# Kernel optimization log

Hardware: AMD Instinct MI355X
Metric: run time of the kernel (lower is better)

The kernel has to match this reference:

```python
import jax, jax.numpy as jnp
import numpy as np

DIM = 192
HEADS = 4
EPS = 1e-12  # F.normalize default eps


def setup_inputs() -> dict:
    key = jax.random.key(0)
    ks = jax.random.split(key, 5)
    b, c, h, w = 8, DIM, 128, 128
    x = jax.random.normal(ks[0], (b, c, h, w), dtype=jnp.float32)
    w_qkv = jax.random.normal(ks[1], (3 * DIM, DIM, 1, 1), dtype=jnp.float32) * (1.0 / np.sqrt(DIM))
    w_dw = jax.random.normal(ks[2], (3 * DIM, 1, 3, 3), dtype=jnp.float32) * (1.0 / 3.0)
    w_proj = jax.random.normal(ks[3], (DIM, DIM, 1, 1), dtype=jnp.float32) * (1.0 / np.sqrt(DIM))
    temperature = jnp.ones((HEADS, 1, 1), dtype=jnp.float32)
    return {"x": x, "w_qkv": w_qkv, "w_dw": w_dw, "w_proj": w_proj, "temperature": temperature}


def _conv1x1(x, w):
    # x: [b,c,h,w], w: [o,c,1,1] -> [b,o,h,w]
    return jnp.einsum('bchw,oc->bohw', x, w[:, :, 0, 0])


def _dwconv3x3(x, w):
    # depthwise 3x3, padding=1; x: [b,C,h,w], w: [C,1,3,3]
    C = x.shape[1]
    return jax.lax.conv_general_dilated(
        x, w, window_strides=(1, 1), padding=((1, 1), (1, 1)),
        dimension_numbers=('NCHW', 'OIHW', 'NCHW'), feature_group_count=C)


def _l2norm(x):
    n = jnp.linalg.norm(x, axis=-1, keepdims=True)
    return x / jnp.maximum(n, EPS)


def reference(x, w_qkv, w_dw, w_proj, temperature):
    b, c, h, w = x.shape
    head = HEADS
    ch = c // head  # channels per head
    qkv = _dwconv3x3(_conv1x1(x, w_qkv), w_dw)  # [b, 3c, h, w]
    q, k, v = jnp.split(qkv, 3, axis=1)  # each [b, c, h, w]

    def to_heads(t):
        # b (head ch) h w -> b head h (ch w)
        t = t.reshape(b, head, ch, h, w)
        return t.transpose(0, 1, 3, 2, 4).reshape(b, head, h, ch * w)

    q1 = _l2norm(to_heads(q))
    k1 = _l2norm(to_heads(k))
    v1 = to_heads(v)
    # attn over height dim: [b, head, h, h]
    attn = jax.nn.softmax(jnp.einsum('bhif,bhjf->bhij', q1, k1) * temperature[None], axis=-1)
    out = jnp.einsum('bhij,bhjf->bhif', attn, v1)  # [b, head, h, ch*w]
    # b head h (ch w) -> b (head ch) h w
    out = out.reshape(b, head, h, ch, w).transpose(0, 1, 3, 2, 4).reshape(b, c, h, w)
    return _conv1x1(out, w_proj)
```

## Files before the change

kernel.cpp:

```cpp
#include <hip/hip_runtime.h>
#include <hip/hip_bf16.h>

#define BB 8
#define CC 192
#define C3 576
#define NH 4
#define CH 48
#define HH 128
#define WW 128
#define HW 16384
#define FF 6144

typedef short s16x8 __attribute__((ext_vector_type(8)));
typedef float f32x4 __attribute__((ext_vector_type(4)));

constexpr size_t SPM = 32ull * 128 * 128;

constexpr size_t OFF_XT  = 0;
constexpr size_t SZ_XT   = (size_t)BB * HW * CC * 2;
constexpr size_t OFF_WQ  = OFF_XT + SZ_XT;
constexpr size_t SZ_WQ   = (size_t)C3 * CC * 2;
constexpr size_t OFF_WP  = OFF_WQ + SZ_WQ;
constexpr size_t SZ_WP   = (size_t)CC * CC * 2;
constexpr size_t OFF_RAW = OFF_WP + SZ_WP;
constexpr size_t SZ_RAW  = (size_t)BB * C3 * HW * 2;
constexpr size_t OFF_DW  = OFF_RAW + SZ_RAW;
constexpr size_t OFF_SP  = OFF_DW + SZ_RAW;
constexpr size_t OFF_ATB = OFF_SP + 8 * SPM * 4;
constexpr size_t OFF_RQ  = OFF_ATB + 32ull * 128 * 128 * 2;
constexpr size_t OFF_RK  = OFF_RQ + 32 * 128 * 4;
constexpr size_t OFF_PS  = OFF_SP;

__device__ __forceinline__ short bf16bits(float v) {
  __hip_bfloat16 t = __float2bfloat16(v);
  return *reinterpret_cast<short*>(&t);
}
__device__ __forceinline__ float b2f(short u) {
  union { unsigned int i; float f; } x;
  x.i = ((unsigned int)(unsigned short)u) << 16;
  return x.f;
}

__device__ __forceinline__ void gload16(const void* g, void* l) {
  __builtin_amdgcn_global_load_lds((const __attribute__((address_space(1))) unsigned int*)g,
                                   (__attribute__((address_space(3))) unsigned int*)l, 16, 0, 0);
}

#define VMWAIT(N) asm volatile("s_waitcnt vmcnt(" #N ")" ::: "memory")
__device__ __forceinline__ void vmdrain() { asm volatile("s_waitcnt vmcnt(0)" ::: "memory"); }
__device__ __forceinline__ void ldsbar() {
  asm volatile("s_waitcnt lgkmcnt(0)" ::: "memory");
  __builtin_amdgcn_s_barrier();
}

__global__ __launch_bounds__(256) void k_cvt_t(const float* __restrict__ in,
                                               __hip_bfloat16* __restrict__ outT) {
  const int p0 = blockIdx.x * 64;
  const int c0 = blockIdx.y * 32;
  const int b = blockIdx.z;
  __shared__ float t[32][65];
  const float* ib = in + (size_t)b * CC * HW;
  const int tid = threadIdx.x;
  {
    const int c = tid >> 3, pl = (tid & 7) * 8;
    const float* s = ib + (size_t)(c0 + c) * HW + p0 + pl;
#pragma unroll
    for (int j = 0; j < 8; ++j) t[c][pl + j] = s[j];
  }
  __syncthreads();
  {
    const int pl = tid >> 2, cl = (tid & 3) * 8;
    __hip_bfloat16* d = outT + (size_t)b * HW * CC + (size_t)(p0 + pl) * CC + c0 + cl;
#pragma unroll
    for (int j = 0; j < 8; ++j) d[j] = __float2bfloat16(t[cl + j][pl]);
  }
}

__global__ __launch_bounds__(256) void k_cvt_w2(const float* __restrict__ in1, int n1,
                                                const float* __restrict__ in2, int n2,
                                                __hip_bfloat16* __restrict__ out) {
  const int i = blockIdx.x * 256 + threadIdx.x;
  if (i < n1) out[i] = __float2bfloat16(in1[i]);
  else if (i < n1 + n2) out[i] = __float2bfloat16(in2[i - n1]);
}

__global__ __launch_bounds__(256) void k_gemm(const __hip_bfloat16* __restrict__ xT,
                                              const __hip_bfloat16* __restrict__ Wb,
                                              __hip_bfloat16* __restrict__ out) {
  const int pG = blockIdx.x * 4;
  const int mBase = blockIdx.y * 96;
  const int b = blockIdx.z;
  __shared__ char smem[62976];
  const int tid = threadIdx.x, wave = tid >> 6, lane = tid & 63;
  const int wm = wave >> 1, wn = wave & 1;
  const __hip_bfloat16* xb = xT + (size_t)b * HW * CC;
  char* Bbase = smem + 36864;

#pragma unroll
  for (int it = 0; it < 9; ++it) {
    const int s = it * 256 + tid;
    const int kc = s / 384, ci = s % 384;
    const int row = ci & 15, kg = (ci >> 4) & 3, mf = ci >> 6;
    gload16(Wb + (size_t)(mBase + mf * 16 + row) * CC + kc * 32 + kg * 8,
            smem + it * 4096 + wave * 1024);
  }

  auto stageB = [&](int pt, int kc, int buf) {
    char* Blc = Bbase + buf * 8192;
    const int pBase = (pG + pt) * 128;
#pragma unroll
    for (int is = 0; is < 2; ++is) {
      const int ci = is * 256 + tid;
      const int col = ci & 15, kg = (ci >> 4) & 3, nf = ci >> 6;
      gload16(xb + (size_t)(pBase + nf * 16 + col) * CC + kc * 32 + kg * 8,
              Blc + is * 4096 + wave * 1024);
    }
  };

  short* E = (short*)Bbase;
  const int r0 = (lane >> 4) * 4, cl = lane & 15;

  for (int pt = 0; pt < 4; ++pt) {
    stageB(pt, 0, 0);
    stageB(pt, 1, 1);
    f32x4 acc[3][4] = {};
#pragma unroll
    for (int kc = 0; kc < 6; ++kc) {
      if (kc < 4) stageB(pt, kc + 2, (kc + 2) % 3);
      if (kc < 4) VMWAIT(4);
      else if (kc == 4) VMWAIT(2);
      else VMWAIT(0);
      __builtin_amdgcn_s_barrier();
      char* Alc = smem + kc * 6144;
      char* Blc = Bbase + (kc % 3) * 8192;
      s16x8 a[3], bf[4];
#pragma unroll
      for (int i = 0; i < 3; ++i) a[i] = *(const s16x8*)(Alc + ((wm * 3 + i) << 10) + (lane << 4));
#pragma unroll
      for (int j = 0; j < 4; ++j) bf[j] = *(const s16x8*)(Blc + ((wn * 4 + j) << 10) + (lane << 4));
#pragma unroll
      for (int i = 0; i < 3; ++i)
#pragma unroll
        for (int j = 0; j < 4; ++j)
          acc[i][j] = __builtin_amdgcn_mfma_f32_16x16x32_bf16(a[i], bf[j], acc[i][j], 0, 0, 0);
      __builtin_amdgcn_s_barrier();
    }
#pragma unroll
    for (int i = 0; i < 3; ++i) {
      const int lr = wm * 48 + i * 16 + r0;
#pragma unroll
      for (int j = 0; j < 4; ++j) {
        const int col = (wn * 4 + j) * 16 + cl;
#pragma unroll
        for (int r = 0; r < 4; ++r) E[(lr + r) * 136 + col] = bf16bits(acc[i][j][r]);
      }
    }
    ldsbar();
    __hip_bfloat16* ob = out + (size_t)b * C3 * HW + (pG + pt) * 128;
#pragma unroll
    for (int it = 0; it < 6; ++it) {
      const int vi = it * 256 + tid;
      const int row = vi >> 4, c8 = (vi & 15) * 8;
      const s16x8 v = *(const s16x8*)(E + row * 136 + c8);
      *(s16x8*)(ob + (size_t)(mBase + row) * HW + c8) = v;
    }
    ldsbar();
  }
}

__global__ __launch_bounds__(256) void k_dwconv(const __hip_bfloat16* __restrict__ in,
                                                const float* __restrict__ wdw,
                                                __hip_bfloat16* __restrict__ out,
                                                __hip_bfloat16* __restrict__ vt,
                                                float* __restrict__ psum) {
  const int c = blockIdx.x;
  const int b = blockIdx.z;
  __shared__ __hip_bfloat16 IN[2][34][152];
  __shared__ char TR[8192];
  const int tid = threadIdx.x;
  const __hip_bfloat16* src = in + ((size_t)b * C3 + c) * HW;
  const bool isV = (c >= 2 * CC);
  if (tid < 136) {
    const int bz = tid >= 68, t2 = tid - bz * 68;
    const int r = t2 >> 1, col = (t2 & 1) ? 136 : 0;
    *(s16x8*)(&IN[bz][r][col]) = (s16x8){};
  }
  const float* wp = wdw + c * 9;
  float wgt[9];
#pragma unroll
  for (int q = 0; q < 9; ++q) wgt[q] = wp[q];

  s16x8 ld[3];
  auto loadTile = [&](int h0) {
#pragma unroll
    for (int it = 0; it < 3; ++it) {
      const int vi = it * 256 + tid;
      if (vi < 544) {
        const int r = vi >> 4, w8 = vi & 15;
        const int hg = h0 - 1 + r;
        s16x8 v = {};
        if (hg >= 0 && hg < HH) v = *(const s16x8*)(src + (size_t)hg * WW + w8 * 8);
        ld[it] = v;
      }
    }
  };
  auto writeTile = [&](int buf) {
#pragma unroll
    for (int it = 0; it < 3; ++it) {
      const int vi = it * 256 + tid;
      if (vi < 544) {
        const int r = vi >> 4, w8 = vi & 15;
        *(s16x8*)(&IN[buf][r][8 + w8 * 8]) = ld[it];
      }
    }
  };

  loadTile(0);
  writeTile(0);
  __syncthreads();

  const int hl = tid >> 3, w0 = (tid & 7) * 16;
  for (int t = 0; t < 4; ++t) {
    const int h0 = t * 32;
    const int cur = t & 1;
    if (t < 3) loadTile(h0 + 32);
    float res[16] = {};
#pragma unroll
    for (int dh = 0; dh < 3; ++dh) {
      const __hip_bfloat16* rp = &IN[cur][hl + dh][0];
      const s16x8 v0 = *(const s16x8*)(rp + w0);
      const s16x8 v1 = *(const s16x8*)(rp + w0 + 8);
      const s16x8 v2 = *(const s16x8*)(rp + w0 + 16);
      const s16x8 v3 = *(const s16x8*)(rp + w0 + 24);
      float rv[18];
      rv[0] = b2f(v0[7]);
#pragma unroll
      for (int e = 0; e < 8; ++e) rv[1 + e] = b2f(v1[e]);
#pragma unroll
      for (int e = 0; e < 8; ++e) rv[9 + e] = b2f(v2[e]);
      rv[17] = b2f(v3[0]);
      const float wa = wgt[dh * 3], wb = wgt[dh * 3 + 1], wc = wgt[dh * 3 + 2];
#pragma unroll
      for (int ww = 0; ww < 16; ++ww)
        res[ww] += rv[ww] * wa + rv[ww + 1] * wb + rv[ww + 2] * wc;
    }
    if (!isV) {
      short pk[16];
#pragma unroll
      for (int ww = 0; ww < 16; ++ww) pk[ww] = bf16bits(res[ww]);
      __hip_bfloat16* dst = out + ((size_t)b * C3 + c) * HW + (size_t)(h0 + hl) * WW + w0;
      *(s16x8*)dst = *(const s16x8*)pk;
      *(s16x8*)(dst + 8) = *(const s16x8*)(pk + 8);
      float ss = 0.f;
#pragma unroll
      for (int ww = 0; ww < 16; ++ww) ss += res[ww] * res[ww];
#pragma unroll
      for (int off = 4; off > 0; off >>= 1) ss += __shfl_down(ss, off);
      if ((tid & 7) == 0) psum[((size_t)b * HH + h0 + hl) * 384 + c] = ss;
      if (t < 3) writeTile(cur ^ 1);
      __syncthreads();
    } else {
      const int rel = c - 2 * CC;
      const int hd = rel / CH, ch = rel - hd * CH;
#pragma unroll
      for (int ww = 0; ww < 16; ++ww) {
        const int w = w0 + ww;
        const int blk = ((w << 2) + (hl >> 3)) ^ ((w >> 3) & 3);
        *(short*)(TR + (blk << 4) + ((hl & 7) << 1)) = bf16bits(res[ww]);
      }
      __syncthreads();
      const int w = tid >> 1, hf = tid & 1;
      short ot[16];
#pragma unroll
      for (int j = 0; j < 2; ++j) {
        const int hh = hf * 16 + j * 8;
        const int blk = ((w << 2) + (hh >> 3)) ^ ((w >> 3) & 3);
        *(s16x8*)(ot + j * 8) = *(const s16x8*)(TR + (blk << 4));
      }
      __hip_bfloat16* vd = vt + ((size_t)(b * NH + hd) * FF + (size_t)ch * WW + w) * HH + h0 + hf * 16;
      *(s16x8*)vd = *(const s16x8*)ot;
      *(s16x8*)(vd + 8) = *(const s16x8*)(ot + 8);
      if (t < 3) writeTile(cur ^ 1);
      __syncthreads();
    }
  }
}

__global__ __launch_bounds__(64) void k_norms2(const float* __restrict__ psum,
                                               float* __restrict__ rq, float* __restrict__ rk) {
  const int i = blockIdx.x;
  const int hd = blockIdx.y;
  const int b = blockIdx.z & 7;
  const int which = blockIdx.z >> 3;
  const int lane = threadIdx.x;
  float s = 0.f;
  if (lane < 48) s = psum[((size_t)b * HH + i) * 384 + which * CC + hd * CH + lane];
#pragma unroll
  for (int off = 32; off > 0; off >>= 1) s += __shfl_down(s, off);
  if (lane == 0) {
    const float n = sqrtf(s);
    float* dst = which ? rk : rq;
    dst[(b * NH + hd) * HH + i] = 1.f / fmaxf(n, 1e-12f);
  }
}

__global__ __launch_bounds__(256) void k_qkm(const __hip_bfloat16* __restrict__ dw,
                                             float* __restrict__ sp) {
  const int ks = blockIdx.x;
  const int bh = blockIdx.y;
  const int i0 = blockIdx.z * 64;
  const int b = bh >> 2, hd = bh & 3;
  const __hip_bfloat16* qb = dw + ((size_t)b * C3 + hd * CH) * HW;
  const __hip_bfloat16* kb = dw + ((size_t)b * C3 + CC + hd * CH) * HW;
  __shared__ char smem[36864];
  const int tid = threadIdx.x, wave = tid >> 6, lane = tid & 63;
  const int wm = wave >> 1, wn = wave & 1;
  f32x4 acc[2][4] = {};

  auto stage = [&](int chunk, int buf) {
    const int ch = ks * 6 + (chunk >> 2);
    const int w0 = (chunk & 3) * 32;
    char* Alc = smem + buf * 12288;
    char* Blc = Alc + 4096;
    {
      const int row = tid & 15, kg = (tid >> 4) & 3;
      gload16(qb + (size_t)ch * HW + (i0 + (tid >> 6) * 16 + row) * WW + w0 + kg * 8,
              Alc + wave * 1024);
    }
#pragma unroll
    for (int is = 0; is < 2; ++is) {
      const int ci = is * 256 + tid;
      const int col = ci & 15, kg = (ci >> 4) & 3, nf = ci >> 6;
      gload16(kb + (size_t)ch * HW + (nf * 16 + col) * WW + w0 + kg * 8,
              Blc + is * 4096 + wave * 1024);
    }
  };

  stage(0, 0);
  stage(1, 1);
  for (int chunk = 0; chunk < 24; ++chunk) {
    if (chunk < 22) stage(chunk + 2, (chunk + 2) % 3);
    if (chunk < 22) VMWAIT(6);
    else if (chunk == 22) VMWAIT(3);
    else VMWAIT(0);
    __builtin_amdgcn_s_barrier();
    char* Alc = smem + (chunk % 3) * 12288;
    char* Blc = Alc + 4096;
    s16x8 a[2], bf[4];
#pragma unroll
    for (int i = 0; i < 2; ++i) a[i] = *(const s16x8*)(Alc + ((wm * 2 + i) << 10) + (lane << 4));
#pragma unroll
    for (int j = 0; j < 4; ++j) bf[j] = *(const s16x8*)(Blc + ((wn * 4 + j) << 10) + (lane << 4));
#pragma unroll
    for (int i = 0; i < 2; ++i)
#pragma unroll
      for (int j = 0; j < 4; ++j)
        acc[i][j] = __builtin_amdgcn_mfma_f32_16x16x32_bf16(a[i], bf[j], acc[i][j], 0, 0, 0);
    __builtin_amdgcn_s_barrier();
  }
  float* o = sp + (size_t)ks * SPM + (size_t)bh * HH * HH;
  const int r0 = (lane >> 4) * 4, cl = lane & 15;
#pragma unroll
  for (int i = 0; i < 2; ++i)
#pragma unroll
    for (int j = 0; j < 4; ++j) {
      const int ii = i0 + wm * 32 + i * 16 + r0;
      const int jj = wn * 64 + j * 16 + cl;
#pragma unroll
      for (int r = 0; r < 4; ++r) o[(ii + r) * HH + jj] = acc[i][j][r];
    }
}

__global__ __launch_bounds__(256) void k_softmax(const float* __restrict__ sp,
                                                 const float* __restrict__ rq,
                                                 const float* __restrict__ rk,
                                                 const float* __restrict__ temp,
                                                 __hip_bfloat16* __restrict__ atb) {
  const int wave = threadIdx.x >> 6, lane = threadIdx.x & 63;
  const int i = blockIdx.x * 4 + wave;
  const int bh = blockIdx.y;
  const int hd = bh & 3;
  const size_t rowoff = ((size_t)bh * HH + i) * HH;
  float s0 = 0.f, s1 = 0.f;
#pragma unroll
  for (int ks = 0; ks < 8; ++ks) {
    s0 += sp[ks * SPM + rowoff + lane];
    s1 += sp[ks * SPM + rowoff + lane + 64];
  }
  const float scale = rq[bh * HH + i] * temp[hd];
  s0 *= scale * rk[bh * HH + lane];
  s1 *= scale * rk[bh * HH + lane + 64];
  float m = fmaxf(s0, s1);
#pragma unroll
  for (int off = 32; off > 0; off >>= 1) m = fmaxf(m, __shfl_xor(m, off));
  const float e0 = expf(s0 - m), e1 = expf(s1 - m);
  float ssum = e0 + e1;
#pragma unroll
  for (int off = 32; off > 0; off >>= 1) ssum += __shfl_xor(ssum, off);
  const float inv = 1.f / ssum;
  atb[rowoff + lane] = __float2bfloat16(e0 * inv);
  atb[rowoff + lane + 64] = __float2bfloat16(e1 * inv);
}

__global__ __launch_bounds__(256) void k_pvm(const __hip_bfloat16* __restrict__ atb,
                                             const __hip_bfloat16* __restrict__ vt,
                                             __hip_bfloat16* __restrict__ pvout) {
  const int fs0 = blockIdx.x * 2;
  const int bh = blockIdx.y;
  const __hip_bfloat16* ab = atb + (size_t)bh * HH * HH;
  __shared__ char smem[57344];
  const int tid = threadIdx.x, wave = tid >> 6, lane = tid & 63;
  const int wm = wave >> 1, wn = wave & 1;

#pragma unroll
  for (int it = 0; it < 8; ++it) {
    const int s = it * 256 + tid;
    const int kc = s >> 9, ci = s & 511;
    const int row = ci & 15, kg = (ci >> 4) & 3, mf = ci >> 6;
    gload16(ab + (size_t)(mf * 16 + row) * HH + kc * 32 + kg * 8,
            smem + it * 4096 + wave * 1024);
  }
  char* Bbase = smem + 32768;

  auto stageB = [&](int st, int buf) {
    const int fs = fs0 + (st >> 2);
    const int kj0 = (st & 3) * 32;
    const __hip_bfloat16* vb = vt + ((size_t)bh * FF + fs * 128) * HH;
    char* Blc = Bbase + buf * 8192;
#pragma unroll
    for (int is = 0; is < 2; ++is) {
      const int ci = is * 256 + tid;
      const int col = ci & 15, kg = (ci >> 4) & 3, nf = ci >> 6;
      gload16(vb + (size_t)(nf * 16 + col) * HH + kj0 + kg * 8,
              Blc + is * 4096 + wave * 1024);
    }
  };

  stageB(0, 0);
  stageB(1, 1);
  const int r0 = (lane >> 4) * 4, cl = lane & 15;
  for (int fr = 0; fr < 2; ++fr) {
    f32x4 acc[4][4] = {};
#pragma unroll
    for (int kc = 0; kc < 4; ++kc) {
      const int st = fr * 4 + kc;
      if (st < 6) stageB(st + 2, (st + 2) % 3);
      if (st < 6) VMWAIT(4);
      else if (st == 6) VMWAIT(2);
      else VMWAIT(0);
      __builtin_amdgcn_s_barrier();
      char* Alc = smem + kc * 8192;
      char* Blc = Bbase + (st % 3) * 8192;
      s16x8 a[4], bf[4];
#pragma unroll
      for (int i = 0; i < 4; ++i) a[i] = *(const s16x8*)(Alc + ((wm * 4 + i) << 10) + (lane << 4));
#pragma unroll
      for (int j = 0; j < 4; ++j) bf[j] = *(const s16x8*)(Blc + ((wn * 4 + j) << 10) + (lane << 4));
#pragma unroll
      for (int i = 0; i < 4; ++i)
#pragma unroll
        for (int j = 0; j < 4; ++j)
          acc[i][j] = __builtin_amdgcn_mfma_f32_16x16x32_bf16(a[i], bf[j], acc[i][j], 0, 0, 0);
      __builtin_amdgcn_s_barrier();
    }
    __hip_bfloat16* ob = pvout + (size_t)bh * HH * FF;
    const int fs = fs0 + fr;
#pragma unroll
    for (int i = 0; i < 4; ++i)
#pragma unroll
      for (int j = 0; j < 4; ++j) {
        const int ii = wm * 64 + i * 16 + r0;
        const int f = fs * 128 + (wn * 4 + j) * 16 + cl;
#pragma unroll
        for (int r = 0; r < 4; ++r) ob[(size_t)(ii + r) * FF + f] = __float2bfloat16(acc[i][j][r]);
      }
  }
}

__global__ __launch_bounds__(256) void k_proj(const __hip_bfloat16* __restrict__ pv,
                                              const __hip_bfloat16* __restrict__ Wp,
                                              float* __restrict__ out) {
  const int i = blockIdx.x;
  const int b = blockIdx.y;
  __shared__ __hip_bfloat16 Al[6144];
  __shared__ __hip_bfloat16 Braw[12288];
  __shared__ __hip_bfloat16 Bfrag[4096];
  char* Alc = (char*)Al;
  char* Brc = (char*)Braw;
  char* Bfc = (char*)Bfrag;
  const int tid = threadIdx.x, wave = tid >> 6, lane = tid & 63;
  const int wm = wave >> 1, wn = wave & 1;
  f32x4 acc[6][4] = {};
  for (int hf = 0; hf < 2; ++hf) {
    if (hf) __syncthreads();
#pragma unroll
    for (int it = 0; it < 6; ++it) {
      const int vi = it * 256 + tid;
      const int r = vi >> 4, w8 = vi & 15;
      const int hi = (r >= 48) ? 1 : 0;
      const int hd = hf * 2 + hi, ch = r - hi * 48;
      const s16x8 v = *(const s16x8*)(pv + ((size_t)(b * NH + hd) * HH + i) * FF + ch * 128 + w8 * 8);
      *(s16x8*)(Brc + r * 256 + ((w8 ^ (r & 15)) << 4)) = v;
    }
    __syncthreads();
    for (int kc = 0; kc < 3; ++kc) {
      const int c0 = hf * 96 + kc * 32;
#pragma unroll
      for (int is = 0; is < 3; ++is) {
        const int ci = is * 256 + tid;
        const int row = ci & 15, kg = (ci >> 4) & 3, mf = ci >> 6;
        gload16(Wp + (size_t)(mf * 16 + row) * CC + c0 + kg * 8,
                Alc + is * 4096 + wave * 1024);
      }
#pragma unroll
      for (int it = 0; it < 2; ++it) {
        const int vi = it * 256 + tid;
        const int col = vi & 15, kg = (vi >> 4) & 3, nf = vi >> 6;
        const int w = nf * 16 + col;
        short tmp[8];
#pragma unroll
        for (int e = 0; e < 8; ++e) {
          const int r = (kc * 4 + kg) * 8 + e;
          tmp[e] = *(const short*)(Brc + r * 256 + (((w >> 3) ^ (r & 15)) << 4) + (w & 7) * 2);
        }
        *(s16x8*)(Bfc + ((nf * 64 + kg * 16 + col) << 4)) = *(const s16x8*)tmp;
      }
      vmdrain();
      __syncthreads();
      s16x8 a[6], bf[4];
#pragma unroll
      for (int mi = 0; mi < 6; ++mi)
        a[mi] = *(const s16x8*)(Alc + ((wm * 6 + mi) << 10) + (lane << 4));
#pragma unroll
      for (int j = 0; j < 4; ++j)
        bf[j] = *(const s16x8*)(Bfc + (((wn * 4 + j) * 64 + lane) << 4));
#pragma unroll
      for (int mi = 0; mi < 6; ++mi)
#pragma unroll
        for (int j = 0; j < 4; ++j)
          acc[mi][j] = __builtin_amdgcn_mfma_f32_16x16x32_bf16(a[mi], bf[j], acc[mi][j], 0, 0, 0);
      __syncthreads();
    }
  }
  const int r0 = (lane >> 4) * 4, cl = lane & 15;
#pragma unroll
  for (int mi = 0; mi < 6; ++mi) {
    const int o = (wm * 6 + mi) * 16 + r0;
#pragma unroll
    for (int j = 0; j < 4; ++j) {
      const int w = (wn * 4 + j) * 16 + cl;
      float* dst = out + ((size_t)b * CC + o) * HW + i * 128 + w;
#pragma unroll
      for (int r = 0; r < 4; ++r) dst[(size_t)r * HW] = acc[mi][j][r];
    }
  }
}

extern "C" void kernel_launch(void* const* d_in, const int* in_sizes, int n_in,
                              void* d_out, int out_size, void* d_ws, size_t ws_size,
                              hipStream_t stream) {
  const float* x     = (const float*)d_in[0];
  const float* wqkv  = (const float*)d_in[1];
  const float* wdw   = (const float*)d_in[2];
  const float* wproj = (const float*)d_in[3];
  const float* temp  = (const float*)d_in[4];

  char* ws = (char*)d_ws;
  __hip_bfloat16* xTb    = (__hip_bfloat16*)(ws + OFF_XT);
  __hip_bfloat16* vt     = (__hip_bfloat16*)(ws + OFF_XT);
  __hip_bfloat16* Wq     = (__hip_bfloat16*)(ws + OFF_WQ);
  __hip_bfloat16* Wp     = (__hip_bfloat16*)(ws + OFF_WP);
  __hip_bfloat16* qkvraw = (__hip_bfloat16*)(ws + OFF_RAW);
  __hip_bfloat16* pvout  = (__hip_bfloat16*)(ws + OFF_RAW);
  __hip_bfloat16* qkvdw  = (__hip_bfloat16*)(ws + OFF_DW);
  float* sp    = (float*)(ws + OFF_SP);
  float* psum  = (float*)(ws + OFF_PS);
  __hip_bfloat16* atb = (__hip_bfloat16*)(ws + OFF_ATB);
  float* rq    = (float*)(ws + OFF_RQ);
  float* rk    = (float*)(ws + OFF_RK);

  k_cvt_w2<<<dim3((C3 * CC + CC * CC + 255) / 256), 256, 0, stream>>>(wqkv, C3 * CC, wproj, CC * CC, Wq);
  k_cvt_t<<<dim3(HW / 64, CC / 32, BB), 256, 0, stream>>>(x, xTb);
  k_gemm<<<dim3(HW / 512, C3 / 96, BB), 256, 0, stream>>>(xTb, Wq, qkvraw);
  k_dwconv<<<dim3(C3, 1, BB), 256, 0, stream>>>(qkvraw, wdw, qkvdw, vt, psum);
  k_norms2<<<dim3(HH, NH, 2 * BB), 64, 0, stream>>>(psum, rq, rk);
  k_qkm<<<dim3(8, 32, 2), 256, 0, stream>>>(qkvdw, sp);
  k_softmax<<<dim3(HH / 4, 32), 256, 0, stream>>>(sp, rq, rk, temp, atb);
  k_pvm<<<dim3(24, 32), 256, 0, stream>>>(atb, vt, pvout);
  k_proj<<<dim3(HH, BB), 256, 0, stream>>>(pvout, Wp, (float*)d_out);
}
```

Measured before the change: 259.2 us.

## Shrink GEMM LDS footprint and split dwconv over row tiles per block

The GEMM moves from triple to double buffering of B tiles and writes its epilogue in two halves, reducing shared memory from about 62KB to 52KB so more blocks can fit per CU. The depthwise conv kernel now launches one block per 32-row tile instead of looping over four tiles with software prefetch. This gives four times more blocks and a smaller LDS footprint. In exchange, the GEMM loses a stage of prefetch depth and the conv loses its load/compute overlap inside each block, and halo rows are reloaded from global memory.

```diff
diff --git a/kernel.cpp b/kernel.cpp
--- a/kernel.cpp
+++ b/kernel.cpp
@@ -90,7 +90,7 @@
   const int pG = blockIdx.x * 4;
   const int mBase = blockIdx.y * 96;
   const int b = blockIdx.z;
-  __shared__ char smem[62976];
+  __shared__ char smem[53248];
   const int tid = threadIdx.x, wave = tid >> 6, lane = tid & 63;
   const int wm = wave >> 1, wn = wave & 1;
   const __hip_bfloat16* xb = xT + (size_t)b * HW * CC;
@@ -122,17 +122,15 @@
 
   for (int pt = 0; pt < 4; ++pt) {
     stageB(pt, 0, 0);
-    stageB(pt, 1, 1);
     f32x4 acc[3][4] = {};
 #pragma unroll
     for (int kc = 0; kc < 6; ++kc) {
-      if (kc < 4) stageB(pt, kc + 2, (kc + 2) % 3);
-      if (kc < 4) VMWAIT(4);
-      else if (kc == 4) VMWAIT(2);
+      if (kc < 5) stageB(pt, kc + 1, (kc + 1) & 1);
+      if (kc < 5) VMWAIT(2);
       else VMWAIT(0);
       __builtin_amdgcn_s_barrier();
       char* Alc = smem + kc * 6144;
-      char* Blc = Bbase + (kc % 3) * 8192;
+      char* Blc = Bbase + (kc & 1) * 8192;
       s16x8 a[3], bf[4];
 #pragma unroll
       for (int i = 0; i < 3; ++i) a[i] = *(const s16x8*)(Alc + ((wm * 3 + i) << 10) + (lane << 4));
@@ -145,26 +143,31 @@
           acc[i][j] = __builtin_amdgcn_mfma_f32_16x16x32_bf16(a[i], bf[j], acc[i][j], 0, 0, 0);
       __builtin_amdgcn_s_barrier();
     }
-#pragma unroll
-    for (int i = 0; i < 3; ++i) {
-      const int lr = wm * 48 + i * 16 + r0;
-#pragma unroll
-      for (int j = 0; j < 4; ++j) {
-        const int col = (wn * 4 + j) * 16 + cl;
-#pragma unroll
-        for (int r = 0; r < 4; ++r) E[(lr + r) * 136 + col] = bf16bits(acc[i][j][r]);
+    __hip_bfloat16* ob = out + (size_t)b * C3 * HW + (pG + pt) * 128;
+#pragma unroll
+    for (int half = 0; half < 2; ++half) {
+      if (wm == half) {
+#pragma unroll
+        for (int i = 0; i < 3; ++i) {
+          const int lr = i * 16 + r0;
+#pragma unroll
+          for (int j = 0; j < 4; ++j) {
+            const int col = (wn * 4 + j) * 16 + cl;
+#pragma unroll
+            for (int r = 0; r < 4; ++r) E[(lr + r) * 136 + col] = bf16bits(acc[i][j][r]);
+          }
+        }
       }
-    }
-    ldsbar();
-    __hip_bfloat16* ob = out + (size_t)b * C3 * HW + (pG + pt) * 128;
-#pragma unroll
-    for (int it = 0; it < 6; ++it) {
-      const int vi = it * 256 + tid;
-      const int row = vi >> 4, c8 = (vi & 15) * 8;
-      const s16x8 v = *(const s16x8*)(E + row * 136 + c8);
-      *(s16x8*)(ob + (size_t)(mBase + row) * HW + c8) = v;
-    }
-    ldsbar();
+      ldsbar();
+#pragma unroll
+      for (int it = 0; it < 3; ++it) {
+        const int vi = it * 256 + tid;
+        const int row = vi >> 4, c8 = (vi & 15) * 8;
+        const s16x8 v = *(const s16x8*)(E + row * 136 + c8);
+        *(s16x8*)(ob + (size_t)(mBase + half * 48 + row) * HW + c8) = v;
+      }
+      ldsbar();
+    }
   }
 }
 
@@ -173,116 +176,89 @@
                                                 __hip_bfloat16* __restrict__ out,
                                                 __hip_bfloat16* __restrict__ vt,
                                                 float* __restrict__ psum) {
-  const int c = blockIdx.x;
+  const int h0 = blockIdx.x * 32;
+  const int c = blockIdx.y;
   const int b = blockIdx.z;
-  __shared__ __hip_bfloat16 IN[2][34][152];
+  __shared__ __hip_bfloat16 IN[34][152];
   __shared__ char TR[8192];
   const int tid = threadIdx.x;
   const __hip_bfloat16* src = in + ((size_t)b * C3 + c) * HW;
-  const bool isV = (c >= 2 * CC);
-  if (tid < 136) {
-    const int bz = tid >= 68, t2 = tid - bz * 68;
-    const int r = t2 >> 1, col = (t2 & 1) ? 136 : 0;
-    *(s16x8*)(&IN[bz][r][col]) = (s16x8){};
+  if (tid < 68) {
+    const int r = tid >> 1, col = (tid & 1) ? 136 : 0;
+    *(s16x8*)(&IN[r][col]) = (s16x8){};
+  }
+#pragma unroll
+  for (int it = 0; it < 3; ++it) {
+    const int vi = it * 256 + tid;
+    if (vi < 544) {
+      const int r = vi >> 4, w8 = vi & 15;
+      const int hg = h0 - 1 + r;
+      s16x8 v = {};
+      if (hg >= 0 && hg < HH) v = *(const s16x8*)(src + (size_t)hg * WW + w8 * 8);
+      *(s16x8*)(&IN[r][8 + w8 * 8]) = v;
+    }
   }
   const float* wp = wdw + c * 9;
   float wgt[9];
 #pragma unroll
   for (int q = 0; q < 9; ++q) wgt[q] = wp[q];
-
-  s16x8 ld[3];
-  auto loadTile = [&](int h0) {
-#pragma unroll
-    for (int it = 0; it < 3; ++it) {
-      const int vi = it * 256 + tid;
-      if (vi < 544) {
-        const int r = vi >> 4, w8 = vi & 15;
-        const int hg = h0 - 1 + r;
-        s16x8 v = {};
-        if (hg >= 0 && hg < HH) v = *(const s16x8*)(src + (size_t)hg * WW + w8 * 8);
-        ld[it] = v;
-      }
-    }
-  };
-  auto writeTile = [&](int buf) {
-#pragma unroll
-    for (int it = 0; it < 3; ++it) {
-      const int vi = it * 256 + tid;
-      if (vi < 544) {
-        const int r = vi >> 4, w8 = vi & 15;
-        *(s16x8*)(&IN[buf][r][8 + w8 * 8]) = ld[it];
-      }
-    }
-  };
-
-  loadTile(0);
-  writeTile(0);
   __syncthreads();
 
   const int hl = tid >> 3, w0 = (tid & 7) * 16;
-  for (int t = 0; t < 4; ++t) {
-    const int h0 = t * 32;
-    const int cur = t & 1;
-    if (t < 3) loadTile(h0 + 32);
-    float res[16] = {};
-#pragma unroll
-    for (int dh = 0; dh < 3; ++dh) {
-      const __hip_bfloat16* rp = &IN[cur][hl + dh][0];
-      const s16x8 v0 = *(const s16x8*)(rp + w0);
-      const s16x8 v1 = *(const s16x8*)(rp + w0 + 8);
-      const s16x8 v2 = *(const s16x8*)(rp + w0 + 16);
-      const s16x8 v3 = *(const s16x8*)(rp + w0 + 24);
-      float rv[18];
-      rv[0] = b2f(v0[7]);
-#pragma unroll
-      for (int e = 0; e < 8; ++e) rv[1 + e] = b2f(v1[e]);
-#pragma unroll
-      for (int e = 0; e < 8; ++e) rv[9 + e] = b2f(v2[e]);
-      rv[17] = b2f(v3[0]);
-      const float wa = wgt[dh * 3], wb = wgt[dh * 3 + 1], wc = wgt[dh * 3 + 2];
-#pragma unroll
-      for (int ww = 0; ww < 16; ++ww)
-        res[ww] += rv[ww] * wa + rv[ww + 1] * wb + rv[ww + 2] * wc;
-    }
-    if (!isV) {
-      short pk[16];
-#pragma unroll
-      for (int ww = 0; ww < 16; ++ww) pk[ww] = bf16bits(res[ww]);
-      __hip_bfloat16* dst = out + ((size_t)b * C3 + c) * HW + (size_t)(h0 + hl) * WW + w0;
-      *(s16x8*)dst = *(const s16x8*)pk;
-      *(s16x8*)(dst + 8) = *(const s16x8*)(pk + 8);
-      float ss = 0.f;
-#pragma unroll
-      for (int ww = 0; ww < 16; ++ww) ss += res[ww] * res[ww];
-#pragma unroll
-      for (int off = 4; off > 0; off >>= 1) ss += __shfl_down(ss, off);
-      if ((tid & 7) == 0) psum[((size_t)b * HH + h0 + hl) * 384 + c] = ss;
-      if (t < 3) writeTile(cur ^ 1);
-      __syncthreads();
-    } else {
-      const int rel = c - 2 * CC;
-      const int hd = rel / CH, ch = rel - hd * CH;
-#pragma unroll
-      for (int ww = 0; ww < 16; ++ww) {
-        const int w = w0 + ww;
-        const int blk = ((w << 2) + (hl >> 3)) ^ ((w >> 3) & 3);
-        *(short*)(TR + (blk << 4) + ((hl & 7) << 1)) = bf16bits(res[ww]);
-      }
-      __syncthreads();
-      const int w = tid >> 1, hf = tid & 1;
-      short ot[16];
-#pragma unroll
-      for (int j = 0; j < 2; ++j) {
-        const int hh = hf * 16 + j * 8;
-        const int blk = ((w << 2) + (hh >> 3)) ^ ((w >> 3) & 3);
-        *(s16x8*)(ot + j * 8) = *(const s16x8*)(TR + (blk << 4));
-      }
-      __hip_bfloat16* vd = vt + ((size_t)(b * NH + hd) * FF + (size_t)ch * WW + w) * HH + h0 + hf * 16;
-      *(s16x8*)vd = *(const s16x8*)ot;
-      *(s16x8*)(vd + 8) = *(const s16x8*)(ot + 8);
-      if (t < 3) writeTile(cur ^ 1);
-      __syncthreads();
-    }
+  float res[16] = {};
+#pragma unroll
+  for (int dh = 0; dh < 3; ++dh) {
+    const __hip_bfloat16* rp = &IN[hl + dh][0];
+    const s16x8 v0 = *(const s16x8*)(rp + w0);
+    const s16x8 v1 = *(const s16x8*)(rp + w0 + 8);
+    const s16x8 v2 = *(const s16x8*)(rp + w0 + 16);
+    const s16x8 v3 = *(const s16x8*)(rp + w0 + 24);
+    float rv[18];
+    rv[0] = b2f(v0[7]);
+#pragma unroll
+    for (int e = 0; e < 8; ++e) rv[1 + e] = b2f(v1[e]);
+#pragma unroll
+    for (int e = 0; e < 8; ++e) rv[9 + e] = b2f(v2[e]);
+    rv[17] = b2f(v3[0]);
+    const float wa = wgt[dh * 3], wb = wgt[dh * 3 + 1], wc = wgt[dh * 3 + 2];
+#pragma unroll
+    for (int ww = 0; ww < 16; ++ww)
+      res[ww] += rv[ww] * wa + rv[ww + 1] * wb + rv[ww + 2] * wc;
+  }
+  if (c < 2 * CC) {
+    short pk[16];
+#pragma unroll
+    for (int ww = 0; ww < 16; ++ww) pk[ww] = bf16bits(res[ww]);
+    __hip_bfloat16* dst = out + ((size_t)b * C3 + c) * HW + (size_t)(h0 + hl) * WW + w0;
+    *(s16x8*)dst = *(const s16x8*)pk;
+    *(s16x8*)(dst + 8) = *(const s16x8*)(pk + 8);
+    float ss = 0.f;
+#pragma unroll
+    for (int ww = 0; ww < 16; ++ww) ss += res[ww] * res[ww];
+#pragma unroll
+    for (int off = 4; off > 0; off >>= 1) ss += __shfl_down(ss, off);
+    if ((tid & 7) == 0) psum[((size_t)b * HH + h0 + hl) * 384 + c] = ss;
+  } else {
+    const int rel = c - 2 * CC;
+    const int hd = rel / CH, ch = rel - hd * CH;
+#pragma unroll
+    for (int ww = 0; ww < 16; ++ww) {
+      const int w = w0 + ww;
+      const int blk = ((w << 2) + (hl >> 3)) ^ ((w >> 3) & 3);
+      *(short*)(TR + (blk << 4) + ((hl & 7) << 1)) = bf16bits(res[ww]);
+    }
+    __syncthreads();
+    const int w = tid >> 1, hf = tid & 1;
+    short ot[16];
+#pragma unroll
+    for (int j = 0; j < 2; ++j) {
+      const int hh = hf * 16 + j * 8;
+      const int blk = ((w << 2) + (hh >> 3)) ^ ((w >> 3) & 3);
+      *(s16x8*)(ot + j * 8) = *(const s16x8*)(TR + (blk << 4));
+    }
+    __hip_bfloat16* vd = vt + ((size_t)(b * NH + hd) * FF + (size_t)ch * WW + w) * HH + h0 + hf * 16;
+    *(s16x8*)vd = *(const s16x8*)ot;
+    *(s16x8*)(vd + 8) = *(const s16x8*)(ot + 8);
   }
 }
 
@@ -582,7 +558,7 @@
   k_cvt_w2<<<dim3((C3 * CC + CC * CC + 255) / 256), 256, 0, stream>>>(wqkv, C3 * CC, wproj, CC * CC, Wq);
   k_cvt_t<<<dim3(HW / 64, CC / 32, BB), 256, 0, stream>>>(x, xTb);
   k_gemm<<<dim3(HW / 512, C3 / 96, BB), 256, 0, stream>>>(xTb, Wq, qkvraw);
-  k_dwconv<<<dim3(C3, 1, BB), 256, 0, stream>>>(qkvraw, wdw, qkvdw, vt, psum);
+  k_dwconv<<<dim3(HH / 32, C3, BB), 256, 0, stream>>>(qkvraw, wdw, qkvdw, vt, psum);
   k_norms2<<<dim3(HH, NH, 2 * BB), 64, 0, stream>>>(psum, rq, rk);
   k_qkm<<<dim3(8, 32, 2), 256, 0, stream>>>(qkvdw, sp);
   k_softmax<<<dim3(HH / 4, 32), 256, 0, stream>>>(sp, rq, rk, temp, atb);
```

New measurement: 256.3 us. No clear change (-1.1%).
